# Kernel optimization log

Hardware: AMD Instinct MI355X
Metric: run time of the kernel (lower is better)

## Reference

```python
import jax, jax.numpy as jnp
import numpy as np

T, B, IN_DIM = 1024, 8, 512
D_VALUE, D_KEY = 64, 64
V_TH = 1.0
EPS = 1e-08


def setup_inputs() -> dict:
    key = jax.random.key(0)
    ks = jax.random.split(key, 7)
    s_in = 1.0 / np.sqrt(IN_DIM)
    x = jax.random.normal(ks[0], (T, B, IN_DIM), dtype=jnp.float32)
    Wv = jax.random.uniform(ks[1], (D_VALUE, IN_DIM), jnp.float32, -s_in, s_in)
    bv = jax.random.uniform(ks[2], (D_VALUE,), jnp.float32, -s_in, s_in)
    Wk = jax.random.uniform(ks[3], (D_KEY, IN_DIM), jnp.float32, -s_in, s_in)
    bk = jax.random.uniform(ks[4], (D_KEY,), jnp.float32, -s_in, s_in)
    Wa = jax.random.uniform(ks[5], (D_KEY, IN_DIM), jnp.float32, -s_in, s_in)
    ba = jax.random.uniform(ks[6], (D_KEY,), jnp.float32, -s_in, s_in)
    return {"x": x, "Wv": Wv, "bv": bv, "Wk": Wk, "bk": bk, "Wa": Wa, "ba": ba}


def reference(x, Wv, bv, Wk, bk, Wa, ba):
    # projections: v (T,B,d), k (T,B,n), alpha (T,B,n)
    v = jnp.einsum('tbi,di->tbd', x, Wv) + bv
    k = jnp.einsum('tbi,ni->tbn', x, Wk) + bk
    alpha = jax.nn.sigmoid(jnp.einsum('tbi,ni->tbn', x, Wa) + ba)
    # outer-product writes: (T,B,d,n)
    writes = jnp.einsum('tbd,tbn->tbdn', v, k)
    # closed-form linear recurrence S_t = S_{t-1} * alpha_t + writes_t via cumprod/cumsum
    P = jnp.cumprod(alpha, axis=0)                       # (T,B,n)
    invP = 1.0 / (P + EPS)
    scaled = writes * invP[:, :, None, :]                # (T,B,d,n)
    S = jnp.cumsum(scaled, axis=0) * P[:, :, None, :]    # (T,B,d,n)
    Tt, Bb = x.shape[0], x.shape[1]
    mem = S.reshape(Tt, Bb, D_VALUE * D_KEY)
    spk = (mem > V_TH).astype(mem.dtype)
    return spk, mem
```

## Files before the change

### kernel.cpp

```cpp
#include <hip/hip_runtime.h>
#include <cmath>

#define TT 1024
#define BB 8
#define IND 512
#define NCH 32
#define CHL 32
#define EPSV 1e-8
#define OUTHALF ((size_t)TT * BB * 4096)

__global__ __launch_bounds__(256)
void k1_proj(const float* __restrict__ x,
             const float* __restrict__ Wv, const float* __restrict__ bv,
             const float* __restrict__ Wk, const float* __restrict__ bk,
             const float* __restrict__ Wa, const float* __restrict__ ba,
             float* __restrict__ vOut, float* __restrict__ kOut,
             float* __restrict__ aOut)
{
    __shared__ float sWt[64][192];
    __shared__ float sXt[64][16];
    const int tid = threadIdx.x;
    const int rowbase = blockIdx.x * 16;
    const int c0 = tid & 63;
    const int r0 = (tid >> 6) << 2;
    double a0[4] = {}, a1[4] = {}, a2[4] = {};

    for (int ko = 0; ko < IND; ko += 64) {
        __syncthreads();
        if (tid < 192) {
            const float* src = (tid < 64  ? Wv + (size_t)tid * IND
                              : tid < 128 ? Wk + (size_t)(tid - 64) * IND
                              :             Wa + (size_t)(tid - 128) * IND) + ko;
            #pragma unroll
            for (int q = 0; q < 64; q += 4) {
                float4 w4 = *(const float4*)(src + q);
                sWt[q+0][tid] = w4.x; sWt[q+1][tid] = w4.y;
                sWt[q+2][tid] = w4.z; sWt[q+3][tid] = w4.w;
            }
        }
        {
            int r  = tid & 15;
            int kq = (tid >> 4) << 2;
            float4 x4 = *(const float4*)(x + (size_t)(rowbase + r) * IND + ko + kq);
            sXt[kq+0][r] = x4.x; sXt[kq+1][r] = x4.y;
            sXt[kq+2][r] = x4.z; sXt[kq+3][r] = x4.w;
        }
        __syncthreads();

        float f0[4] = {}, f1[4] = {}, f2[4] = {};
        #pragma unroll
        for (int q = 0; q < 64; ++q) {
            float4 xv = *(const float4*)&sXt[q][r0];
            float w0 = sWt[q][c0], w1 = sWt[q][c0 + 64], w2 = sWt[q][c0 + 128];
            f0[0] = fmaf(xv.x, w0, f0[0]); f1[0] = fmaf(xv.x, w1, f1[0]); f2[0] = fmaf(xv.x, w2, f2[0]);
            f0[1] = fmaf(xv.y, w0, f0[1]); f1[1] = fmaf(xv.y, w1, f1[1]); f2[1] = fmaf(xv.y, w2, f2[1]);
            f0[2] = fmaf(xv.z, w0, f0[2]); f1[2] = fmaf(xv.z, w1, f1[2]); f2[2] = fmaf(xv.z, w2, f2[2]);
            f0[3] = fmaf(xv.w, w0, f0[3]); f1[3] = fmaf(xv.w, w1, f1[3]); f2[3] = fmaf(xv.w, w2, f2[3]);
        }
        #pragma unroll
        for (int i = 0; i < 4; ++i) { a0[i] += f0[i]; a1[i] += f1[i]; a2[i] += f2[i]; }
    }

    #pragma unroll
    for (int i = 0; i < 4; ++i) {
        int r = rowbase + r0 + i;
        vOut[r * 64 + c0] = (float)(a0[i] + (double)bv[c0]);
        kOut[r * 64 + c0] = (float)(a1[i] + (double)bk[c0]);
        double z = a2[i] + (double)ba[c0];
        aOut[r * 64 + c0] = (float)(1.0 / (1.0 + exp(-z)));
    }
}

__global__ __launch_bounds__(256)
void k2a_chunkprod(const float* __restrict__ alpha, double* __restrict__ cpA)
{
    int gt = blockIdx.x * 256 + threadIdx.x;
    int ch = gt >> 9, chain = gt & 511;
    double p = 1.0;
    int base = (ch * CHL) * 512 + chain;
    #pragma unroll
    for (int i = 0; i < CHL; ++i) p *= (double)alpha[base + i * 512];
    cpA[gt] = p;
}

__global__ __launch_bounds__(512)
void k2b_prefix(double* __restrict__ cpA)
{
    int chain = threadIdx.x;
    double vals[NCH];
    #pragma unroll
    for (int ch = 0; ch < NCH; ++ch) vals[ch] = cpA[ch * 512 + chain];
    double run = 1.0;
    #pragma unroll
    for (int ch = 0; ch < NCH; ++ch) {
        cpA[ch * 512 + chain] = run;
        run *= vals[ch];
    }
}

__global__ __launch_bounds__(256)
void k3_csum(const float* __restrict__ vIn, const float* __restrict__ kIn,
             const float* __restrict__ alpha, const double* __restrict__ cpA,
             double* __restrict__ Csum)
{
    __shared__ double sV[CHL * 64];
    const int tid = threadIdx.x;
    const int ch = blockIdx.x >> 3;
    const int b  = blockIdx.x & 7;
    #pragma unroll
    for (int q = 0; q < 8; ++q) {
        int idx = q * 256 + tid;
        int ti = idx >> 6, d = idx & 63;
        sV[idx] = (double)vIn[(((ch * CHL + ti) * BB) + b) * 64 + d];
    }
    __syncthreads();
    const int n = tid & 63;
    const int w = tid >> 6;
    double P = cpA[ch * 512 + b * 64 + n];
    double C[16];
    #pragma unroll
    for (int j = 0; j < 16; ++j) C[j] = 0.0;
    for (int i = 0; i < CHL; ++i) {
        int base = ((ch * CHL + i) * BB + b) * 64 + n;
        P *= (double)alpha[base];
        double invp = 1.0 / (P + EPSV);
        double kd = (double)kIn[base] * invp;
        const double* vrow = &sV[i * 64 + w * 16];
        #pragma unroll
        for (int j = 0; j < 16; ++j) C[j] = fma(vrow[j], kd, C[j]);
    }
    size_t cb = ((size_t)ch * 8 + b) * 4096 + (size_t)w * 1024 + n;
    #pragma unroll
    for (int j = 0; j < 16; ++j) Csum[cb + j * 64] = C[j];
}

__global__ __launch_bounds__(256)
void k3b_prefix(double* __restrict__ Csum)
{
    int s = blockIdx.x * 256 + threadIdx.x;
    int b = s >> 12, rest = s & 4095;
    double vals[NCH];
    #pragma unroll
    for (int ch = 0; ch < NCH; ++ch)
        vals[ch] = Csum[((size_t)ch * 8 + b) * 4096 + rest];
    double run = 0.0;
    #pragma unroll
    for (int ch = 0; ch < NCH; ++ch) {
        Csum[((size_t)ch * 8 + b) * 4096 + rest] = run;
        run += vals[ch];
    }
}

__global__ __launch_bounds__(256)
void k4_scan(const float* __restrict__ vIn, const float* __restrict__ kIn,
             const float* __restrict__ alpha, const double* __restrict__ cpA,
             const double* __restrict__ Csum, float* __restrict__ outp)
{
    __shared__ double sV[CHL * 64];
    const int tid = threadIdx.x;
    const int ch = blockIdx.x >> 3;
    const int b  = blockIdx.x & 7;
    #pragma unroll
    for (int q = 0; q < 8; ++q) {
        int idx = q * 256 + tid;
        int ti = idx >> 6, d = idx & 63;
        sV[idx] = (double)vIn[(((ch * CHL + ti) * BB) + b) * 64 + d];
    }
    __syncthreads();
    const int n = tid & 63;
    const int w = tid >> 6;
    double P = cpA[ch * 512 + b * 64 + n];
    size_t cb = ((size_t)ch * 8 + b) * 4096 + (size_t)w * 1024 + n;
    double C[16];
    #pragma unroll
    for (int j = 0; j < 16; ++j) C[j] = Csum[cb + j * 64];

    float* spk = outp;
    float* mem = outp + OUTHALF;
    for (int i = 0; i < CHL; ++i) {
        int t = ch * CHL + i;
        int base = (t * BB + b) * 64 + n;
        P *= (double)alpha[base];
        double invp = 1.0 / (P + EPSV);
        double kd = (double)kIn[base] * invp;
        const double* vrow = &sV[i * 64 + w * 16];
        size_t ob = ((size_t)t * BB + b) * 4096 + (size_t)w * 1024 + n;
        #pragma unroll
        for (int j = 0; j < 16; ++j) {
            C[j] = fma(vrow[j], kd, C[j]);
            double S = P * C[j];
            mem[ob + j * 64] = (float)S;
            spk[ob + j * 64] = (S > 1.0) ? 1.0f : 0.0f;
        }
    }
}

extern "C" void kernel_launch(void* const* d_in, const int* in_sizes, int n_in,
                              void* d_out, int out_size, void* d_ws, size_t ws_size,
                              hipStream_t stream)
{
    const float* x  = (const float*)d_in[0];
    const float* Wv = (const float*)d_in[1];
    const float* bv = (const float*)d_in[2];
    const float* Wk = (const float*)d_in[3];
    const float* bk = (const float*)d_in[4];
    const float* Wa = (const float*)d_in[5];
    const float* ba = (const float*)d_in[6];
    float* out = (float*)d_out;

    char* ws = (char*)d_ws;
    float*  v     = (float*)(ws);
    float*  kk    = (float*)(ws + (2u << 20));
    float*  alpha = (float*)(ws + (4u << 20));
    double* cpA   = (double*)(ws + (6u << 20));
    double* Csum  = (double*)(ws + (7u << 20));

    hipLaunchKernelGGL(k1_proj,       dim3(512), dim3(256), 0, stream,
                       x, Wv, bv, Wk, bk, Wa, ba, v, kk, alpha);
    hipLaunchKernelGGL(k2a_chunkprod, dim3(64),  dim3(256), 0, stream, alpha, cpA);
    hipLaunchKernelGGL(k2b_prefix,    dim3(1),   dim3(512), 0, stream, cpA);
    hipLaunchKernelGGL(k3_csum,       dim3(256), dim3(256), 0, stream,
                       v, kk, alpha, cpA, Csum);
    hipLaunchKernelGGL(k3b_prefix,    dim3(128), dim3(256), 0, stream, Csum);
    hipLaunchKernelGGL(k4_scan,       dim3(256), dim3(256), 0, stream,
                       v, kk, alpha, cpA, Csum, out);
}
```

Before: 117.8 us.

## Fold chunk prefix scans into consumer kernels, dropping two launches

Removes the two separate prefix-scan kernels, one over chunk products and one over chunk sums. Each block of the csum and scan kernels now rebuilds its own exclusive prefix by looping over all earlier chunks. This saves two kernel launches and the serial single-block launch. In exchange the scan kernel rereads up to 31 chunks of partial state per block, which adds redundant global traffic and work that grows with chunk index.

```diff
diff --git a/kernel.cpp b/kernel.cpp
--- a/kernel.cpp
+++ b/kernel.cpp
@@ -83,21 +83,6 @@
     cpA[gt] = p;
 }
 
-__global__ __launch_bounds__(512)
-void k2b_prefix(double* __restrict__ cpA)
-{
-    int chain = threadIdx.x;
-    double vals[NCH];
-    #pragma unroll
-    for (int ch = 0; ch < NCH; ++ch) vals[ch] = cpA[ch * 512 + chain];
-    double run = 1.0;
-    #pragma unroll
-    for (int ch = 0; ch < NCH; ++ch) {
-        cpA[ch * 512 + chain] = run;
-        run *= vals[ch];
-    }
-}
-
 __global__ __launch_bounds__(256)
 void k3_csum(const float* __restrict__ vIn, const float* __restrict__ kIn,
              const float* __restrict__ alpha, const double* __restrict__ cpA,
@@ -116,7 +101,8 @@
     __syncthreads();
     const int n = tid & 63;
     const int w = tid >> 6;
-    double P = cpA[ch * 512 + b * 64 + n];
+    double P = 1.0;
+    for (int c = 0; c < ch; ++c) P *= cpA[c * 512 + b * 64 + n];
     double C[16];
     #pragma unroll
     for (int j = 0; j < 16; ++j) C[j] = 0.0;
@@ -132,23 +118,6 @@
     size_t cb = ((size_t)ch * 8 + b) * 4096 + (size_t)w * 1024 + n;
     #pragma unroll
     for (int j = 0; j < 16; ++j) Csum[cb + j * 64] = C[j];
-}
-
-__global__ __launch_bounds__(256)
-void k3b_prefix(double* __restrict__ Csum)
-{
-    int s = blockIdx.x * 256 + threadIdx.x;
-    int b = s >> 12, rest = s & 4095;
-    double vals[NCH];
-    #pragma unroll
-    for (int ch = 0; ch < NCH; ++ch)
-        vals[ch] = Csum[((size_t)ch * 8 + b) * 4096 + rest];
-    double run = 0.0;
-    #pragma unroll
-    for (int ch = 0; ch < NCH; ++ch) {
-        Csum[((size_t)ch * 8 + b) * 4096 + rest] = run;
-        run += vals[ch];
-    }
 }
 
 __global__ __launch_bounds__(256)
@@ -169,11 +138,16 @@
     __syncthreads();
     const int n = tid & 63;
     const int w = tid >> 6;
-    double P = cpA[ch * 512 + b * 64 + n];
-    size_t cb = ((size_t)ch * 8 + b) * 4096 + (size_t)w * 1024 + n;
+    double P = 1.0;
+    for (int c = 0; c < ch; ++c) P *= cpA[c * 512 + b * 64 + n];
     double C[16];
     #pragma unroll
-    for (int j = 0; j < 16; ++j) C[j] = Csum[cb + j * 64];
+    for (int j = 0; j < 16; ++j) C[j] = 0.0;
+    for (int c = 0; c < ch; ++c) {
+        size_t cb = ((size_t)c * 8 + b) * 4096 + (size_t)w * 1024 + n;
+        #pragma unroll
+        for (int j = 0; j < 16; ++j) C[j] += Csum[cb + j * 64];
+    }
 
     float* spk = outp;
     float* mem = outp + OUTHALF;
@@ -218,10 +192,8 @@
     hipLaunchKernelGGL(k1_proj,       dim3(512), dim3(256), 0, stream,
                        x, Wv, bv, Wk, bk, Wa, ba, v, kk, alpha);
     hipLaunchKernelGGL(k2a_chunkprod, dim3(64),  dim3(256), 0, stream, alpha, cpA);
-    hipLaunchKernelGGL(k2b_prefix,    dim3(1),   dim3(512), 0, stream, cpA);
     hipLaunchKernelGGL(k3_csum,       dim3(256), dim3(256), 0, stream,
                        v, kk, alpha, cpA, Csum);
-    hipLaunchKernelGGL(k3b_prefix,    dim3(128), dim3(256), 0, stream, Csum);
     hipLaunchKernelGGL(k4_scan,       dim3(256), dim3(256), 0, stream,
                        v, kk, alpha, cpA, Csum, out);
 }
```

New measurement: 138.3 us. +17.4%, slower.

## Restructure projection kernel to stream weights via uniform scalar loads

Applied to the files above, without the earlier changes.

The projection kernel is retiled so each block handles 64 rows and 16 output columns per projection. Weights are read directly from global memory with wave-uniform addresses (scalar loads), and only x is staged in a swizzled shared tile to avoid bank conflicts. The change removes the large transposed weight staging and its strided shared-memory writes, and it uses vectorised float4 output stores. In exchange, x is reloaded by four blocks per row group, and the weight reads depend on scalar cache bandwidth.

```diff
diff --git a/kernel.cpp b/kernel.cpp
--- a/kernel.cpp
+++ b/kernel.cpp
@@ -17,58 +17,81 @@
              float* __restrict__ vOut, float* __restrict__ kOut,
              float* __restrict__ aOut)
 {
-    __shared__ float sWt[64][192];
-    __shared__ float sXt[64][16];
-    const int tid = threadIdx.x;
-    const int rowbase = blockIdx.x * 16;
-    const int c0 = tid & 63;
-    const int r0 = (tid >> 6) << 2;
-    double a0[4] = {}, a1[4] = {}, a2[4] = {};
+    __shared__ float sX[64 * 64];
+    const int tid  = threadIdx.x;
+    const int lane = tid & 63;
+    const int wq   = __builtin_amdgcn_readfirstlane(tid >> 6);
+    const int rb   = (blockIdx.x >> 2) * 64;
+    const int cb   = ((blockIdx.x & 3) << 4) + (wq << 2);
+
+    const float* pWv = Wv + (size_t)cb * IND;
+    const float* pWk = Wk + (size_t)cb * IND;
+    const float* pWa = Wa + (size_t)cb * IND;
+
+    double av[4] = {}, ak[4] = {}, aa[4] = {};
 
     for (int ko = 0; ko < IND; ko += 64) {
         __syncthreads();
-        if (tid < 192) {
-            const float* src = (tid < 64  ? Wv + (size_t)tid * IND
-                              : tid < 128 ? Wk + (size_t)(tid - 64) * IND
-                              :             Wa + (size_t)(tid - 128) * IND) + ko;
+        {
+            int r   = tid >> 2;
+            int kg0 = (tid & 3) << 2;
+            const float* src = x + (size_t)(rb + r) * IND + ko + (kg0 << 2);
             #pragma unroll
-            for (int q = 0; q < 64; q += 4) {
-                float4 w4 = *(const float4*)(src + q);
-                sWt[q+0][tid] = w4.x; sWt[q+1][tid] = w4.y;
-                sWt[q+2][tid] = w4.z; sWt[q+3][tid] = w4.w;
+            for (int j = 0; j < 4; ++j) {
+                float4 v4 = *(const float4*)(src + (j << 2));
+                int pk = (kg0 + j) ^ (r & 7);
+                *(float4*)&sX[(r << 6) + (pk << 2)] = v4;
             }
         }
-        {
-            int r  = tid & 15;
-            int kq = (tid >> 4) << 2;
-            float4 x4 = *(const float4*)(x + (size_t)(rowbase + r) * IND + ko + kq);
-            sXt[kq+0][r] = x4.x; sXt[kq+1][r] = x4.y;
-            sXt[kq+2][r] = x4.z; sXt[kq+3][r] = x4.w;
+        __syncthreads();
+
+        float fv[4] = {}, fk[4] = {}, fa[4] = {};
+        #pragma unroll
+        for (int kg = 0; kg < 16; ++kg) {
+            float4 xv = *(const float4*)&sX[(lane << 6) + (((kg ^ (lane & 7))) << 2)];
+            const int kk = ko + (kg << 2);
+            float4 wv0 = *(const float4*)(pWv + 0 * IND + kk);
+            float4 wv1 = *(const float4*)(pWv + 1 * IND + kk);
+            float4 wv2 = *(const float4*)(pWv + 2 * IND + kk);
+            float4 wv3 = *(const float4*)(pWv + 3 * IND + kk);
+            float4 wk0 = *(const float4*)(pWk + 0 * IND + kk);
+            float4 wk1 = *(const float4*)(pWk + 1 * IND + kk);
+            float4 wk2 = *(const float4*)(pWk + 2 * IND + kk);
+            float4 wk3 = *(const float4*)(pWk + 3 * IND + kk);
+            float4 wa0 = *(const float4*)(pWa + 0 * IND + kk);
+            float4 wa1 = *(const float4*)(pWa + 1 * IND + kk);
+            float4 wa2 = *(const float4*)(pWa + 2 * IND + kk);
+            float4 wa3 = *(const float4*)(pWa + 3 * IND + kk);
+            fv[0]=fmaf(xv.x,wv0.x,fv[0]); fv[0]=fmaf(xv.y,wv0.y,fv[0]); fv[0]=fmaf(xv.z,wv0.z,fv[0]); fv[0]=fmaf(xv.w,wv0.w,fv[0]);
+            fv[1]=fmaf(xv.x,wv1.x,fv[1]); fv[1]=fmaf(xv.y,wv1.y,fv[1]); fv[1]=fmaf(xv.z,wv1.z,fv[1]); fv[1]=fmaf(xv.w,wv1.w,fv[1]);
+            fv[2]=fmaf(xv.x,wv2.x,fv[2]); fv[2]=fmaf(xv.y,wv2.y,fv[2]); fv[2]=fmaf(xv.z,wv2.z,fv[2]); fv[2]=fmaf(xv.w,wv2.w,fv[2]);
+            fv[3]=fmaf(xv.x,wv3.x,fv[3]); fv[3]=fmaf(xv.y,wv3.y,fv[3]); fv[3]=fmaf(xv.z,wv3.z,fv[3]); fv[3]=fmaf(xv.w,wv3.w,fv[3]);
+            fk[0]=fmaf(xv.x,wk0.x,fk[0]); fk[0]=fmaf(xv.y,wk0.y,fk[0]); fk[0]=fmaf(xv.z,wk0.z,fk[0]); fk[0]=fmaf(xv.w,wk0.w,fk[0]);
+            fk[1]=fmaf(xv.x,wk1.x,fk[1]); fk[1]=fmaf(xv.y,wk1.y,fk[1]); fk[1]=fmaf(xv.z,wk1.z,fk[1]); fk[1]=fmaf(xv.w,wk1.w,fk[1]);
+            fk[2]=fmaf(xv.x,wk2.x,fk[2]); fk[2]=fmaf(xv.y,wk2.y,fk[2]); fk[2]=fmaf(xv.z,wk2.z,fk[2]); fk[2]=fmaf(xv.w,wk2.w,fk[2]);
+            fk[3]=fmaf(xv.x,wk3.x,fk[3]); fk[3]=fmaf(xv.y,wk3.y,fk[3]); fk[3]=fmaf(xv.z,wk3.z,fk[3]); fk[3]=fmaf(xv.w,wk3.w,fk[3]);
+            fa[0]=fmaf(xv.x,wa0.x,fa[0]); fa[0]=fmaf(xv.y,wa0.y,fa[0]); fa[0]=fmaf(xv.z,wa0.z,fa[0]); fa[0]=fmaf(xv.w,wa0.w,fa[0]);
+            fa[1]=fmaf(xv.x,wa1.x,fa[1]); fa[1]=fmaf(xv.y,wa1.y,fa[1]); fa[1]=fmaf(xv.z,wa1.z,fa[1]); fa[1]=fmaf(xv.w,wa1.w,fa[1]);
+            fa[2]=fmaf(xv.x,wa2.x,fa[2]); fa[2]=fmaf(xv.y,wa2.y,fa[2]); fa[2]=fmaf(xv.z,wa2.z,fa[2]); fa[2]=fmaf(xv.w,wa2.w,fa[2]);
+            fa[3]=fmaf(xv.x,wa3.x,fa[3]); fa[3]=fmaf(xv.y,wa3.y,fa[3]); fa[3]=fmaf(xv.z,wa3.z,fa[3]); fa[3]=fmaf(xv.w,wa3.w,fa[3]);
         }
-        __syncthreads();
-
-        float f0[4] = {}, f1[4] = {}, f2[4] = {};
-        #pragma unroll
-        for (int q = 0; q < 64; ++q) {
-            float4 xv = *(const float4*)&sXt[q][r0];
-            float w0 = sWt[q][c0], w1 = sWt[q][c0 + 64], w2 = sWt[q][c0 + 128];
-            f0[0] = fmaf(xv.x, w0, f0[0]); f1[0] = fmaf(xv.x, w1, f1[0]); f2[0] = fmaf(xv.x, w2, f2[0]);
-            f0[1] = fmaf(xv.y, w0, f0[1]); f1[1] = fmaf(xv.y, w1, f1[1]); f2[1] = fmaf(xv.y, w2, f2[1]);
-            f0[2] = fmaf(xv.z, w0, f0[2]); f1[2] = fmaf(xv.z, w1, f1[2]); f2[2] = fmaf(xv.z, w2, f2[2]);
-            f0[3] = fmaf(xv.w, w0, f0[3]); f1[3] = fmaf(xv.w, w1, f1[3]); f2[3] = fmaf(xv.w, w2, f2[3]);
-        }
-        #pragma unroll
-        for (int i = 0; i < 4; ++i) { a0[i] += f0[i]; a1[i] += f1[i]; a2[i] += f2[i]; }
-    }
-
-    #pragma unroll
-    for (int i = 0; i < 4; ++i) {
-        int r = rowbase + r0 + i;
-        vOut[r * 64 + c0] = (float)(a0[i] + (double)bv[c0]);
-        kOut[r * 64 + c0] = (float)(a1[i] + (double)bk[c0]);
-        double z = a2[i] + (double)ba[c0];
-        aOut[r * 64 + c0] = (float)(1.0 / (1.0 + exp(-z)));
-    }
+        #pragma unroll
+        for (int c = 0; c < 4; ++c) { av[c] += fv[c]; ak[c] += fk[c]; aa[c] += fa[c]; }
+    }
+
+    const size_t row = (size_t)rb + lane;
+    float4 vo, ko4, ao;
+    vo.x  = (float)(av[0] + (double)bv[cb+0]); vo.y  = (float)(av[1] + (double)bv[cb+1]);
+    vo.z  = (float)(av[2] + (double)bv[cb+2]); vo.w  = (float)(av[3] + (double)bv[cb+3]);
+    ko4.x = (float)(ak[0] + (double)bk[cb+0]); ko4.y = (float)(ak[1] + (double)bk[cb+1]);
+    ko4.z = (float)(ak[2] + (double)bk[cb+2]); ko4.w = (float)(ak[3] + (double)bk[cb+3]);
+    ao.x = (float)(1.0 / (1.0 + exp(-(aa[0] + (double)ba[cb+0]))));
+    ao.y = (float)(1.0 / (1.0 + exp(-(aa[1] + (double)ba[cb+1]))));
+    ao.z = (float)(1.0 / (1.0 + exp(-(aa[2] + (double)ba[cb+2]))));
+    ao.w = (float)(1.0 / (1.0 + exp(-(aa[3] + (double)ba[cb+3]))));
+    *(float4*)&vOut[row * 64 + cb] = vo;
+    *(float4*)&kOut[row * 64 + cb] = ko4;
+    *(float4*)&aOut[row * 64 + cb] = ao;
 }
 
 __global__ __launch_bounds__(256)
```

Result: slower. 151.5 us (+28.6%).
